# Performance work log

Hardware: AMD Instinct MI355X
Metric: run time of the kernel (lower is better)

Reference implementation:

```python
import jax, jax.numpy as jnp
import numpy as np

D_MODEL = 1024
NUM_HEADS = 16
HEAD_DIM = D_MODEL // NUM_HEADS
B, T = 4, 2048


def setup_inputs() -> dict:
    key = jax.random.key(0)
    ks = jax.random.split(key, 6)
    s = 1.0 / np.sqrt(D_MODEL)  # ~ nn.Linear init scale
    return {
        "x_q": jax.random.normal(ks[0], (B, T, D_MODEL), jnp.float32),
        "x_kv": jax.random.normal(ks[1], (B, T, D_MODEL), jnp.float32),
        "Wq": jax.random.uniform(ks[2], (D_MODEL, D_MODEL), jnp.float32, -s, s),
        "Wk": jax.random.uniform(ks[3], (D_MODEL, D_MODEL), jnp.float32, -s, s),
        "Wv": jax.random.uniform(ks[4], (D_MODEL, D_MODEL), jnp.float32, -s, s),
        "Wo": jax.random.uniform(ks[5], (D_MODEL, D_MODEL), jnp.float32, -s, s),
    }


def reference(x_q, x_kv, Wq, Wk, Wv, Wo):
    Bq, Tq, C = x_q.shape
    Tk = x_kv.shape[1]
    # torch nn.Linear: y = x @ W.T
    q = (x_q @ Wq.T).reshape(Bq, Tq, NUM_HEADS, HEAD_DIM).transpose(0, 2, 1, 3)
    k = (x_kv @ Wk.T).reshape(Bq, Tk, NUM_HEADS, HEAD_DIM).transpose(0, 2, 1, 3)
    v = (x_kv @ Wv.T).reshape(Bq, Tk, NUM_HEADS, HEAD_DIM).transpose(0, 2, 1, 3)
    scores = jnp.einsum("bhqd,bhkd->bhqk", q, k) / jnp.sqrt(
        jnp.asarray(HEAD_DIM, x_q.dtype)
    )
    causal = jnp.triu(jnp.ones((Tq, Tk), bool), k=1)  # True above diagonal
    scores = jnp.where(causal, -jnp.inf, scores)
    attn = jax.nn.softmax(scores, axis=-1)
    out = jnp.einsum("bhqk,bhkd->bhqd", attn, v)
    out = out.transpose(0, 2, 1, 3).reshape(Bq, Tq, C)
    return out @ Wo.T
```

## Files before the change

kernel.cpp:

```cpp
#include <hip/hip_runtime.h>
#include <stdint.h>

#define T_SEQ 2048
#define NH 16
#define HD 64
#define DM 1024
#define BB 4
#define MROWS (BB * T_SEQ)

typedef __attribute__((ext_vector_type(8))) __bf16 bf16x8;
typedef __attribute__((ext_vector_type(8))) unsigned short u16x8;
typedef __attribute__((ext_vector_type(4))) unsigned short u16x4;
typedef __attribute__((ext_vector_type(4))) float f32x4;

__device__ __forceinline__ unsigned short f2bf(float f) {
  return __builtin_bit_cast(unsigned short, (__bf16)f);
}

__device__ __forceinline__ bf16x8 ld8_f32(const float* __restrict__ p) {
  f32x4 a = *(const f32x4*)p;
  f32x4 b = *(const f32x4*)(p + 4);
  u16x8 u;
#pragma unroll
  for (int i = 0; i < 4; ++i) {
    u[i]     = f2bf(a[i]);
    u[i + 4] = f2bf(b[i]);
  }
  return __builtin_bit_cast(bf16x8, u);
}

__device__ __forceinline__ bf16x8 ld8_bf(const unsigned short* p) {
  return __builtin_bit_cast(bf16x8, *(const u16x8*)p);
}

__device__ __forceinline__ bf16x8 ld8_lds(const unsigned short* p) {
  u16x4 a = *(const u16x4*)p;
  u16x4 b = *(const u16x4*)(p + 4);
  return __builtin_bit_cast(bf16x8,
      __builtin_shufflevector(a, b, 0, 1, 2, 3, 4, 5, 6, 7));
}

__device__ __forceinline__ u16x4 lo4(u16x8 v) {
  return __builtin_shufflevector(v, v, 0, 1, 2, 3);
}
__device__ __forceinline__ u16x4 hi4(u16x8 v) {
  return __builtin_shufflevector(v, v, 4, 5, 6, 7);
}

__device__ __forceinline__ void gload_lds16(const unsigned short* g,
                                            unsigned short* l) {
  __builtin_amdgcn_global_load_lds(
      (const __attribute__((address_space(1))) unsigned int*)g,
      (__attribute__((address_space(3))) unsigned int*)l, 16, 0, 0);
}

__global__ __launch_bounds__(256) void conv_f32_bf16(
    const float* __restrict__ src, unsigned short* __restrict__ dst, int n8) {
  const int i = blockIdx.x * 256 + threadIdx.x;
  if (i < n8)
    *(u16x8*)(dst + (size_t)i * 8) =
        __builtin_bit_cast(u16x8, ld8_f32(src + (size_t)i * 8));
}

__global__ __launch_bounds__(256) void conv_w4(
    const float* __restrict__ s0, const float* __restrict__ s1,
    const float* __restrict__ s2, const float* __restrict__ s3,
    unsigned short* __restrict__ d012, unsigned short* __restrict__ d3,
    int n8) {
  const int y = blockIdx.y;
  const float* src = (y == 0) ? s0 : (y == 1) ? s1 : (y == 2) ? s2 : s3;
  unsigned short* dst = (y < 3) ? d012 + (size_t)y * DM * DM : d3;
  const int i = blockIdx.x * 256 + threadIdx.x;
  if (i < n8)
    *(u16x8*)(dst + (size_t)i * 8) =
        __builtin_bit_cast(u16x8, ld8_f32(src + (size_t)i * 8));
}

template <int MODE>
__global__ __launch_bounds__(256) void gemm128(
    const unsigned short* __restrict__ A, const unsigned short* __restrict__ B,
    void* __restrict__ Cv, void* __restrict__ Cv2, int M, int N, int K) {
  __shared__ __align__(16) unsigned short As[2][2][128 * 32];
  __shared__ __align__(16) unsigned short Bs[2][2][128 * 32];

  const int t = threadIdx.x;
  const int lane = t & 63, wave = t >> 6;
  const int lin = (int)(blockIdx.x + gridDim.x * blockIdx.y);
  const int nx = N >> 7;
  const int mpx = (M >> 7) >> 3;
  const int xcd = lin & 7, slot = lin >> 3;
  const int m0 = (xcd * mpx + slot / nx) * 128;
  const int n0 = (slot % nx) * 128;

  const int srow = t >> 2;
  const int scol = (t & 3) * 8;
  const unsigned short* ga0 = A + (size_t)(m0 + srow) * K + scol;
  const unsigned short* ga1 = A + (size_t)(m0 + 64 + srow) * K + scol;
  const unsigned short* gb0 = B + (size_t)(n0 + srow) * K + scol;
  const unsigned short* gb1 = B + (size_t)(n0 + 64 + srow) * K + scol;
  const int lo0 = (wave * 16) * 32, lo1 = (64 + wave * 16) * 32;

  const int mw = (wave >> 1) * 64, nw = (wave & 1) * 64;
  const int fr = lane & 15, fq = (lane >> 4) * 8;

  f32x4 acc[4][4];
#pragma unroll
  for (int i = 0; i < 4; ++i)
#pragma unroll
    for (int j = 0; j < 4; ++j) acc[i][j] = (f32x4){0.f, 0.f, 0.f, 0.f};

  auto stage = [&](int buf, int k0) {
    gload_lds16(ga0 + k0,      &As[buf][0][lo0]);
    gload_lds16(ga1 + k0,      &As[buf][0][lo1]);
    gload_lds16(gb0 + k0,      &Bs[buf][0][lo0]);
    gload_lds16(gb1 + k0,      &Bs[buf][0][lo1]);
    gload_lds16(ga0 + k0 + 32, &As[buf][1][lo0]);
    gload_lds16(ga1 + k0 + 32, &As[buf][1][lo1]);
    gload_lds16(gb0 + k0 + 32, &Bs[buf][1][lo0]);
    gload_lds16(gb1 + k0 + 32, &Bs[buf][1][lo1]);
  };

  stage(0, 0);
  __syncthreads();

  const int NT = K >> 6;
  int cur = 0;
  for (int kt = 0; kt < NT; ++kt) {
    if (kt + 1 < NT) stage(cur ^ 1, (kt + 1) << 6);
#pragma unroll
    for (int ks = 0; ks < 2; ++ks) {
      bf16x8 af[4], bfr[4];
#pragma unroll
      for (int i = 0; i < 4; ++i)
        af[i] = ld8_bf(&As[cur][ks][(mw + i * 16 + fr) * 32 + fq]);
#pragma unroll
      for (int j = 0; j < 4; ++j)
        bfr[j] = ld8_bf(&Bs[cur][ks][(nw + j * 16 + fr) * 32 + fq]);
#pragma unroll
      for (int i = 0; i < 4; ++i)
#pragma unroll
        for (int j = 0; j < 4; ++j)
          acc[i][j] = __builtin_amdgcn_mfma_f32_16x16x32_bf16(
              af[i], bfr[j], acc[i][j], 0, 0, 0);
    }
    __syncthreads();
    cur ^= 1;
  }

  const int orow = (lane >> 4) * 4, ocol = lane & 15;
  const bool kv_lo = (MODE == 3) && (n0 < DM);
#pragma unroll
  for (int i = 0; i < 4; ++i)
#pragma unroll
    for (int j = 0; j < 4; ++j) {
      if constexpr (MODE == 2) {
        const int mb = m0 + mw + i * 16 + orow;
        const int n = n0 + nw + j * 16 + ocol;
        u16x4 pk;
#pragma unroll
        for (int r = 0; r < 4; ++r) pk[r] = f2bf(acc[i][j][r]);
        unsigned short* dst = (unsigned short*)Cv +
            ((size_t)((mb >> 11) * NH + (n >> 6)) * HD + (n & 63)) * T_SEQ +
            (mb & 2047);
        *(u16x4*)dst = pk;
      } else if constexpr (MODE == 3) {
        const int mb = m0 + mw + i * 16 + orow;
        const int n = n0 + nw + j * 16 + ocol;
        if (kv_lo) {
#pragma unroll
          for (int r = 0; r < 4; ++r)
            ((unsigned short*)Cv)[(size_t)(mb + r) * DM + n] =
                f2bf(acc[i][j][r]);
        } else {
          const int nv = n - DM;
          u16x4 pk;
#pragma unroll
          for (int r = 0; r < 4; ++r) pk[r] = f2bf(acc[i][j][r]);
          unsigned short* dst = (unsigned short*)Cv2 +
              ((size_t)((mb >> 11) * NH + (nv >> 6)) * HD + (nv & 63)) *
                  T_SEQ +
              (mb & 2047);
          *(u16x4*)dst = pk;
        }
      } else {
#pragma unroll
        for (int r = 0; r < 4; ++r) {
          const size_t idx = (size_t)(m0 + mw + i * 16 + orow + r) * N +
                             (n0 + nw + j * 16 + ocol);
          if constexpr (MODE == 1)
            ((float*)Cv)[idx] = acc[i][j][r];
          else
            ((unsigned short*)Cv)[idx] = f2bf(acc[i][j][r]);
        }
      }
    }
}

#define ASTR 68

__global__ __launch_bounds__(256, 2) void attn_flash2(
    const unsigned short* Qw, const unsigned short* __restrict__ Kw,
    const unsigned short* __restrict__ Vt, unsigned short* Ow) {
  __shared__ __align__(16) unsigned short k_lds[2][64][ASTR];
  __shared__ __align__(16) unsigned short vt_lds[2][64][ASTR];
  __shared__ __align__(16) unsigned short p_lds[4][32][ASTR];
  __shared__ float alpha_lds[4][32];
  __shared__ float l_lds[4][32];

  const int tid = threadIdx.x, lane = tid & 63, wave = tid >> 6;
  const int c16 = lane & 15, quad = lane >> 4;
  const int b = blockIdx.z, h = blockIdx.y;
  const int pi = blockIdx.x;
  const int qb0A = (15 - pi) * 128;
  const int qb0B = pi * 128;
  const size_t rkbase = (size_t)b * T_SEQ * DM + (size_t)h * HD;
  const size_t vtbase = (size_t)(b * NH + h) * HD * T_SEQ;

  const int q_loA = qb0A + wave * 32;
  const int q_loB = qb0B + wave * 32;

  bf16x8 qfA[2][2], qfB[2][2];
#pragma unroll
  for (int nf = 0; nf < 2; ++nf) {
    const unsigned short* qpA =
        Qw + rkbase + (size_t)(q_loA + nf * 16 + c16) * DM + quad * 8;
    qfA[nf][0] = ld8_bf(qpA);
    qfA[nf][1] = ld8_bf(qpA + 32);
    const unsigned short* qpB =
        Qw + rkbase + (size_t)(q_loB + nf * 16 + c16) * DM + quad * 8;
    qfB[nf][0] = ld8_bf(qpB);
    qfB[nf][1] = ld8_bf(qpB + 32);
  }

  f32x4 oA[2][4], oB[2][4];
#pragma unroll
  for (int nf = 0; nf < 2; ++nf)
#pragma unroll
    for (int j = 0; j < 4; ++j) {
      oA[nf][j] = (f32x4){0.f, 0.f, 0.f, 0.f};
      oB[nf][j] = (f32x4){0.f, 0.f, 0.f, 0.f};
    }
  float mA[2] = {-3.0e38f, -3.0e38f}, lA[2] = {0.f, 0.f};
  float mB[2] = {-3.0e38f, -3.0e38f}, lB[2] = {0.f, 0.f};

  const int srow = tid >> 2;
  const int scol = (tid & 3) * 16;
  const int ntiles = (qb0A + 191) >> 6;
  const int ntA_w = (q_loA + 95) >> 6;
  const int ntB_w = (q_loB + 95) >> 6;

  const unsigned short* kp0 = Kw + rkbase + (size_t)srow * DM + scol;
  const unsigned short* vp0 = Vt + vtbase + (size_t)srow * T_SEQ + scol;

  auto subtile = [&](const bf16x8 (&qf)[2][2], f32x4 (&o)[2][4],
                     float (&m_r)[2], float (&l_r)[2], const int q_lo,
                     const int kb0, const int bi) {
    f32x4 s[4][2];
    __builtin_amdgcn_s_setprio(1);
#pragma unroll
    for (int mf = 0; mf < 4; ++mf) {
      const unsigned short* kr = &k_lds[bi][mf * 16 + c16][quad * 8];
      const bf16x8 k0 = ld8_lds(kr);
      const bf16x8 k1 = ld8_lds(kr + 32);
#pragma unroll
      for (int nf = 0; nf < 2; ++nf) {
        f32x4 a = {0.f, 0.f, 0.f, 0.f};
        a = __builtin_amdgcn_mfma_f32_16x16x32_bf16(k0, qf[nf][0], a, 0, 0, 0);
        a = __builtin_amdgcn_mfma_f32_16x16x32_bf16(k1, qf[nf][1], a, 0, 0, 0);
        s[mf][nf] = a;
      }
    }
    __builtin_amdgcn_s_setprio(0);
    if (kb0 + 63 > q_lo) {
#pragma unroll
      for (int mf = 0; mf < 4; ++mf) {
        const int key0 = kb0 + mf * 16 + quad * 4;
#pragma unroll
        for (int nf = 0; nf < 2; ++nf) {
          const int qg = q_lo + nf * 16 + c16;
#pragma unroll
          for (int r = 0; r < 4; ++r)
            s[mf][nf][r] =
                (key0 + r <= qg) ? s[mf][nf][r] * 0.125f : -3.0e38f;
        }
      }
    } else {
#pragma unroll
      for (int mf = 0; mf < 4; ++mf)
#pragma unroll
        for (int nf = 0; nf < 2; ++nf)
#pragma unroll
          for (int r = 0; r < 4; ++r) s[mf][nf][r] *= 0.125f;
    }

#pragma unroll
    for (int nf = 0; nf < 2; ++nf) {
      float mx = -3.0e38f;
#pragma unroll
      for (int mf = 0; mf < 4; ++mf)
#pragma unroll
        for (int r = 0; r < 4; ++r) mx = fmaxf(mx, s[mf][nf][r]);
      mx = fmaxf(mx, __shfl_xor(mx, 16, 64));
      mx = fmaxf(mx, __shfl_xor(mx, 32, 64));
      const float m_new = fmaxf(m_r[nf], mx);
      const float al = __expf(m_r[nf] - m_new);
      m_r[nf] = m_new;
      float ps = 0.f;
#pragma unroll
      for (int mf = 0; mf < 4; ++mf) {
        u16x4 pk;
#pragma unroll
        for (int r = 0; r < 4; ++r) {
          const float e = __expf(s[mf][nf][r] - m_new);
          ps += e;
          pk[r] = f2bf(e);
        }
        *(u16x4*)&p_lds[wave][nf * 16 + c16][mf * 16 + quad * 4] = pk;
      }
      ps += __shfl_xor(ps, 16, 64);
      ps += __shfl_xor(ps, 32, 64);
      l_r[nf] = l_r[nf] * al + ps;
      if (quad == 0) alpha_lds[wave][nf * 16 + c16] = al;
    }
    __threadfence_block();

#pragma unroll
    for (int nf = 0; nf < 2; ++nf) {
      float alr[4];
#pragma unroll
      for (int r = 0; r < 4; ++r)
        alr[r] = alpha_lds[wave][nf * 16 + quad * 4 + r];
#pragma unroll
      for (int j = 0; j < 4; ++j)
#pragma unroll
        for (int r = 0; r < 4; ++r) o[nf][j][r] *= alr[r];
    }

    bf16x8 pf[2][2];
#pragma unroll
    for (int nf = 0; nf < 2; ++nf) {
      const unsigned short* pw = &p_lds[wave][nf * 16 + c16][quad * 8];
      pf[nf][0] = ld8_lds(pw);
      pf[nf][1] = ld8_lds(pw + 32);
    }
    __builtin_amdgcn_s_setprio(1);
#pragma unroll
    for (int j = 0; j < 4; ++j) {
      const unsigned short* vr = &vt_lds[bi][j * 16 + c16][quad * 8];
      const bf16x8 v0 = ld8_lds(vr);
      const bf16x8 v1 = ld8_lds(vr + 32);
#pragma unroll
      for (int nf = 0; nf < 2; ++nf) {
        o[nf][j] = __builtin_amdgcn_mfma_f32_16x16x32_bf16(pf[nf][0], v0,
                                                           o[nf][j], 0, 0, 0);
        o[nf][j] = __builtin_amdgcn_mfma_f32_16x16x32_bf16(pf[nf][1], v1,
                                                           o[nf][j], 0, 0, 0);
      }
    }
    __builtin_amdgcn_s_setprio(0);
  };

  {
    u16x8 ka = *(const u16x8*)kp0;
    u16x8 kc = *(const u16x8*)(kp0 + 8);
    u16x8 va = *(const u16x8*)vp0;
    u16x8 vc = *(const u16x8*)(vp0 + 8);
    *(u16x4*)&k_lds[0][srow][scol]       = lo4(ka);
    *(u16x4*)&k_lds[0][srow][scol + 4]   = hi4(ka);
    *(u16x4*)&k_lds[0][srow][scol + 8]   = lo4(kc);
    *(u16x4*)&k_lds[0][srow][scol + 12]  = hi4(kc);
    *(u16x4*)&vt_lds[0][srow][scol]      = lo4(va);
    *(u16x4*)&vt_lds[0][srow][scol + 4]  = hi4(va);
    *(u16x4*)&vt_lds[0][srow][scol + 8]  = lo4(vc);
    *(u16x4*)&vt_lds[0][srow][scol + 12] = hi4(vc);
  }
  __syncthreads();

  int cur = 0;
  for (int t = 0; t < ntiles; ++t) {
    const int kb0 = t * 64;
    const bool pf = (t + 1 < ntiles);
    u16x8 ka, kc, va, vc;
    if (pf) {
      const unsigned short* kp = kp0 + (size_t)(kb0 + 64) * DM;
      ka = *(const u16x8*)kp;
      kc = *(const u16x8*)(kp + 8);
      const unsigned short* vp = vp0 + (kb0 + 64);
      va = *(const u16x8*)vp;
      vc = *(const u16x8*)(vp + 8);
    }
    if (t < ntA_w) subtile(qfA, oA, mA, lA, q_loA, kb0, cur);
    if (t < ntB_w) subtile(qfB, oB, mB, lB, q_loB, kb0, cur);
    if (pf) {
      const int nb = cur ^ 1;
      *(u16x4*)&k_lds[nb][srow][scol]       = lo4(ka);
      *(u16x4*)&k_lds[nb][srow][scol + 4]   = hi4(ka);
      *(u16x4*)&k_lds[nb][srow][scol + 8]   = lo4(kc);
      *(u16x4*)&k_lds[nb][srow][scol + 12]  = hi4(kc);
      *(u16x4*)&vt_lds[nb][srow][scol]      = lo4(va);
      *(u16x4*)&vt_lds[nb][srow][scol + 4]  = hi4(va);
      *(u16x4*)&vt_lds[nb][srow][scol + 8]  = lo4(vc);
      *(u16x4*)&vt_lds[nb][srow][scol + 12] = hi4(vc);
      __syncthreads();
      cur = nb;
    }
  }

  auto epi = [&](f32x4 (&o)[2][4], float (&l_r)[2], const int q_lo) {
    if (quad == 0) {
      l_lds[wave][c16] = l_r[0];
      l_lds[wave][16 + c16] = l_r[1];
    }
    __threadfence_block();
#pragma unroll
    for (int nf = 0; nf < 2; ++nf)
#pragma unroll
      for (int r = 0; r < 4; ++r) {
        const int qg = q_lo + nf * 16 + quad * 4 + r;
        const float inv = 1.0f / l_lds[wave][nf * 16 + quad * 4 + r];
        unsigned short* orow = Ow + rkbase + (size_t)qg * DM;
#pragma unroll
        for (int j = 0; j < 4; ++j)
          orow[j * 16 + c16] = f2bf(o[nf][j][r] * inv);
      }
  };
  epi(oA, lA, q_loA);
  __threadfence_block();
  epi(oB, lB, q_loB);
}

extern "C" void kernel_launch(void* const* d_in, const int* in_sizes, int n_in,
                              void* d_out, int out_size, void* d_ws, size_t ws_size,
                              hipStream_t stream) {
  const float* x_q  = (const float*)d_in[0];
  const float* x_kv = (const float*)d_in[1];
  const float* Wq   = (const float*)d_in[2];
  const float* Wk   = (const float*)d_in[3];
  const float* Wv   = (const float*)d_in[4];
  const float* Wo   = (const float*)d_in[5];
  float* out = (float*)d_out;

  unsigned short* scr  = (unsigned short*)d_out;
  unsigned short* Sx   = scr;
  unsigned short* Wk_b = scr + (size_t)MROWS * DM;
  unsigned short* Wv_b = Wk_b + (size_t)DM * DM;
  unsigned short* Wq_b = Wv_b + (size_t)DM * DM;

  unsigned short* qb   = (unsigned short*)d_ws;
  unsigned short* kb   = qb + (size_t)MROWS * DM;
  unsigned short* vtb  = kb + (size_t)MROWS * DM;
  unsigned short* Wo_b = vtb + (size_t)MROWS * DM;

  const int nW8 = DM * DM / 8;
  const int nX8 = MROWS * DM / 8;

  conv_w4<<<dim3(nW8 / 256, 4), 256, 0, stream>>>(Wk, Wv, Wq, Wo, Wk_b, Wo_b,
                                                  nW8);
  conv_f32_bf16<<<nX8 / 256, 256, 0, stream>>>(x_kv, Sx, nX8);

  gemm128<3><<<dim3(2 * DM / 128, MROWS / 128), 256, 0, stream>>>(
      Sx, Wk_b, kb, vtb, MROWS, 2 * DM, DM);
  conv_f32_bf16<<<nX8 / 256, 256, 0, stream>>>(x_q, Sx, nX8);
  gemm128<0><<<dim3(DM / 128, MROWS / 128), 256, 0, stream>>>(
      Sx, Wq_b, qb, nullptr, MROWS, DM, DM);
  attn_flash2<<<dim3(8, NH, BB), 256, 0, stream>>>(qb, kb, vtb, qb);
  gemm128<1><<<dim3(DM / 128, MROWS / 128), 256, 0, stream>>>(
      qb, Wo_b, out, nullptr, MROWS, DM, DM);
}
```

Measured before the change: 295.8 us.

## Fold softmax scale into Q projection, use exp2 with lazy rescale, fuse conversions

The Q projection epilogue now multiplies by scale*log2(e), so the attention kernel drops its per-score scaling and uses exp2f. Running-max rescaling of the output accumulator is skipped unless the max grows by more than 8 in any lane, and the alpha and l values move through lane shuffles instead of LDS. The weight and x_kv fp32-to-bf16 conversions are merged into one launch. The lazy rescale lets exponentials reach up to 2^8 before the bf16 P is formed, which changes rounding slightly, and the Q values are rounded to bf16 after scaling.

```diff
diff --git a/kernel.cpp b/kernel.cpp
--- a/kernel.cpp
+++ b/kernel.cpp
@@ -8,6 +8,8 @@
 #define BB 4
 #define MROWS (BB * T_SEQ)
 
+#define QSCALE 0.18033688011112042f
+
 typedef __attribute__((ext_vector_type(8))) __bf16 bf16x8;
 typedef __attribute__((ext_vector_type(8))) unsigned short u16x8;
 typedef __attribute__((ext_vector_type(4))) unsigned short u16x4;
@@ -62,18 +64,25 @@
         __builtin_bit_cast(u16x8, ld8_f32(src + (size_t)i * 8));
 }
 
-__global__ __launch_bounds__(256) void conv_w4(
-    const float* __restrict__ s0, const float* __restrict__ s1,
-    const float* __restrict__ s2, const float* __restrict__ s3,
-    unsigned short* __restrict__ d012, unsigned short* __restrict__ d3,
-    int n8) {
-  const int y = blockIdx.y;
-  const float* src = (y == 0) ? s0 : (y == 1) ? s1 : (y == 2) ? s2 : s3;
-  unsigned short* dst = (y < 3) ? d012 + (size_t)y * DM * DM : d3;
-  const int i = blockIdx.x * 256 + threadIdx.x;
-  if (i < n8)
+__global__ __launch_bounds__(256) void conv_stage1(
+    const float* __restrict__ Wk, const float* __restrict__ Wv,
+    const float* __restrict__ Wq, const float* __restrict__ Wo,
+    const float* __restrict__ xkv, unsigned short* __restrict__ Wkb012,
+    unsigned short* __restrict__ Wob, unsigned short* __restrict__ Sx) {
+  const int bid = blockIdx.x;
+  const int WSEG = (DM * DM / 8) / 256;
+  if (bid < 4 * WSEG) {
+    const int w = bid >> 9;
+    const float* src = (w == 0) ? Wk : (w == 1) ? Wv : (w == 2) ? Wq : Wo;
+    unsigned short* dst = (w < 3) ? Wkb012 + (size_t)w * DM * DM : Wob;
+    const int i = (bid & (WSEG - 1)) * 256 + threadIdx.x;
     *(u16x8*)(dst + (size_t)i * 8) =
         __builtin_bit_cast(u16x8, ld8_f32(src + (size_t)i * 8));
+  } else {
+    const int i = (bid - 4 * WSEG) * 256 + threadIdx.x;
+    *(u16x8*)(Sx + (size_t)i * 8) =
+        __builtin_bit_cast(u16x8, ld8_f32(xkv + (size_t)i * 8));
+  }
 }
 
 template <int MODE>
@@ -187,10 +196,12 @@
         for (int r = 0; r < 4; ++r) {
           const size_t idx = (size_t)(m0 + mw + i * 16 + orow + r) * N +
                              (n0 + nw + j * 16 + ocol);
+          float v = acc[i][j][r];
+          if constexpr (MODE == 4) v *= QSCALE;
           if constexpr (MODE == 1)
-            ((float*)Cv)[idx] = acc[i][j][r];
+            ((float*)Cv)[idx] = v;
           else
-            ((unsigned short*)Cv)[idx] = f2bf(acc[i][j][r]);
+            ((unsigned short*)Cv)[idx] = f2bf(v);
         }
       }
     }
@@ -204,8 +215,6 @@
   __shared__ __align__(16) unsigned short k_lds[2][64][ASTR];
   __shared__ __align__(16) unsigned short vt_lds[2][64][ASTR];
   __shared__ __align__(16) unsigned short p_lds[4][32][ASTR];
-  __shared__ float alpha_lds[4][32];
-  __shared__ float l_lds[4][32];
 
   const int tid = threadIdx.x, lane = tid & 63, wave = tid >> 6;
   const int c16 = lane & 15, quad = lane >> 4;
@@ -280,17 +289,9 @@
           const int qg = q_lo + nf * 16 + c16;
 #pragma unroll
           for (int r = 0; r < 4; ++r)
-            s[mf][nf][r] =
-                (key0 + r <= qg) ? s[mf][nf][r] * 0.125f : -3.0e38f;
+            if (key0 + r > qg) s[mf][nf][r] = -3.0e38f;
         }
       }
-    } else {
-#pragma unroll
-      for (int mf = 0; mf < 4; ++mf)
-#pragma unroll
-        for (int nf = 0; nf < 2; ++nf)
-#pragma unroll
-          for (int r = 0; r < 4; ++r) s[mf][nf][r] *= 0.125f;
     }
 
 #pragma unroll
@@ -302,16 +303,26 @@
         for (int r = 0; r < 4; ++r) mx = fmaxf(mx, s[mf][nf][r]);
       mx = fmaxf(mx, __shfl_xor(mx, 16, 64));
       mx = fmaxf(mx, __shfl_xor(mx, 32, 64));
-      const float m_new = fmaxf(m_r[nf], mx);
-      const float al = __expf(m_r[nf] - m_new);
-      m_r[nf] = m_new;
+      if (!__all(mx - m_r[nf] <= 8.0f)) {
+        const float m_new = fmaxf(m_r[nf], mx);
+        const float al = exp2f(m_r[nf] - m_new);
+        m_r[nf] = m_new;
+        l_r[nf] *= al;
+        float alr[4];
+#pragma unroll
+        for (int r = 0; r < 4; ++r) alr[r] = __shfl(al, quad * 4 + r, 16);
+#pragma unroll
+        for (int j = 0; j < 4; ++j)
+#pragma unroll
+          for (int r = 0; r < 4; ++r) o[nf][j][r] *= alr[r];
+      }
       float ps = 0.f;
 #pragma unroll
       for (int mf = 0; mf < 4; ++mf) {
         u16x4 pk;
 #pragma unroll
         for (int r = 0; r < 4; ++r) {
-          const float e = __expf(s[mf][nf][r] - m_new);
+          const float e = exp2f(s[mf][nf][r] - m_r[nf]);
           ps += e;
           pk[r] = f2bf(e);
         }
@@ -319,22 +330,9 @@
       }
       ps += __shfl_xor(ps, 16, 64);
       ps += __shfl_xor(ps, 32, 64);
-      l_r[nf] = l_r[nf] * al + ps;
-      if (quad == 0) alpha_lds[wave][nf * 16 + c16] = al;
+      l_r[nf] += ps;
     }
     __threadfence_block();
-
-#pragma unroll
-    for (int nf = 0; nf < 2; ++nf) {
-      float alr[4];
-#pragma unroll
-      for (int r = 0; r < 4; ++r)
-        alr[r] = alpha_lds[wave][nf * 16 + quad * 4 + r];
-#pragma unroll
-      for (int j = 0; j < 4; ++j)
-#pragma unroll
-        for (int r = 0; r < 4; ++r) o[nf][j][r] *= alr[r];
-    }
 
     bf16x8 pf[2][2];
 #pragma unroll
@@ -407,17 +405,12 @@
   }
 
   auto epi = [&](f32x4 (&o)[2][4], float (&l_r)[2], const int q_lo) {
-    if (quad == 0) {
-      l_lds[wave][c16] = l_r[0];
-      l_lds[wave][16 + c16] = l_r[1];
-    }
-    __threadfence_block();
 #pragma unroll
     for (int nf = 0; nf < 2; ++nf)
 #pragma unroll
       for (int r = 0; r < 4; ++r) {
         const int qg = q_lo + nf * 16 + quad * 4 + r;
-        const float inv = 1.0f / l_lds[wave][nf * 16 + quad * 4 + r];
+        const float inv = 1.0f / __shfl(l_r[nf], quad * 4 + r, 16);
         unsigned short* orow = Ow + rkbase + (size_t)qg * DM;
 #pragma unroll
         for (int j = 0; j < 4; ++j)
@@ -425,7 +418,6 @@
       }
   };
   epi(oA, lA, q_loA);
-  __threadfence_block();
   epi(oB, lB, q_loB);
 }
 
@@ -453,15 +445,15 @@
 
   const int nW8 = DM * DM / 8;
   const int nX8 = MROWS * DM / 8;
-
-  conv_w4<<<dim3(nW8 / 256, 4), 256, 0, stream>>>(Wk, Wv, Wq, Wo, Wk_b, Wo_b,
-                                                  nW8);
-  conv_f32_bf16<<<nX8 / 256, 256, 0, stream>>>(x_kv, Sx, nX8);
+  (void)Wv_b;
+
+  conv_stage1<<<4 * (nW8 / 256) + nX8 / 256, 256, 0, stream>>>(
+      Wk, Wv, Wq, Wo, x_kv, Wk_b, Wo_b, Sx);
 
   gemm128<3><<<dim3(2 * DM / 128, MROWS / 128), 256, 0, stream>>>(
       Sx, Wk_b, kb, vtb, MROWS, 2 * DM, DM);
   conv_f32_bf16<<<nX8 / 256, 256, 0, stream>>>(x_q, Sx, nX8);
-  gemm128<0><<<dim3(DM / 128, MROWS / 128), 256, 0, stream>>>(
+  gemm128<4><<<dim3(DM / 128, MROWS / 128), 256, 0, stream>>>(
       Sx, Wq_b, qb, nullptr, MROWS, DM, DM);
   attn_flash2<<<dim3(8, NH, BB), 256, 0, stream>>>(qb, kb, vtb, qb);
   gemm128<1><<<dim3(DM / 128, MROWS / 128), 256, 0, stream>>>(
```

New measurement: 294.5 us. About the same (-0.4%).
